# Performance work log

Measured on AMD Instinct MI355X. Metric: run time of the kernel, lower is better.

## Reference

```python
import jax, jax.numpy as jnp
import numpy as np
from jax import lax

NUM_CLASSES = 19
B, H, W = 4, 512, 512
IGNORE = 255
BLOCK = 16
MAX_N_RATIO = 0.01
LB_SMOOTH = 0.2
MAX_CLIP_DIST = 20.0
BORDER_FACTOR = 0.1
MAX_DIS = 1e5

# ---------- setup helpers (numpy, exact EDT matching scipy distance_transform_edt) ----------

def _edt(mask):
    """Exact Euclidean distance to nearest True pixel. mask: (H,W) bool."""
    Hm, Wm = mask.shape
    INF = 1e6
    g = np.where(mask, 0.0, INF).astype(np.float32)
    for j in range(1, Wm):
        g[:, j] = np.minimum(g[:, j], g[:, j - 1] + 1.0)
    for j in range(Wm - 2, -1, -1):
        g[:, j] = np.minimum(g[:, j], g[:, j + 1] + 1.0)
    gg = g * g  # (H,W) squared 1D row distances
    rows = np.arange(Hm, dtype=np.float32)
    out = np.empty((Hm, Wm), np.float32)
    CH = 64
    for s in range(0, Hm, CH):
        d2 = (rows[s:s + CH, None] - rows[None, :]) ** 2  # (CH,H)
        out[s:s + CH] = np.sqrt(np.min(d2[:, :, None] + gg[None, :, :], axis=1))
    return out


def _dist_maps(targets):
    """Replicates gtruth2boundary + dist_map_transform + relu(-dist): relu(EDT_to_boundary - 1)."""
    t = targets[:, 0]
    ud = np.zeros(t.shape, bool)
    lr = np.zeros(t.shape, bool)
    ud[:, :-1] = (t[:, 1:] - t[:, :-1]) != 0
    lr[:, :, :-1] = (t[:, :, 1:] - t[:, :, :-1]) != 0
    bnd = ud | lr | (t == IGNORE)
    out = np.zeros(t.shape, np.float32)
    for i in range(t.shape[0]):
        if bnd[i].any():
            out[i] = np.maximum(_edt(bnd[i]) - 1.0, 0.0)
    return out[:, None]  # (B,1,H,W)


def setup_inputs():
    key = jax.random.key(0)
    k1, k2 = jax.random.split(key)
    slices = jax.random.normal(k1, (B, NUM_CLASSES, H, W), jnp.float32)
    low = np.asarray(jax.random.randint(k2, (B, 1, H // BLOCK, W // BLOCK), 0, NUM_CLASSES))
    tgt = np.repeat(np.repeat(low, BLOCK, 2), BLOCK, 3).astype(np.int32)
    dist_maps = jnp.asarray(_dist_maps(tgt))
    return {"slices": slices, "dist_maps": dist_maps, "targets": jnp.asarray(tgt)}


# neighbor offset order from the torch code; index 8 is the center
_DX = [1, -1, 0, 0, -1, 1, -1, 1, 0]
_DY = [0, 0, -1, 1, 1, 1, -1, -1, 0]


def reference(slices, dist_maps, targets):
    Bc, C, Hc, Wc = slices.shape
    x = jnp.transpose(slices, (0, 2, 3, 1))               # (B,H,W,C)
    lsm = jax.nn.log_softmax(x, axis=-1)
    sm = jnp.exp(lsm)

    # ---- slices2boundary: per-pixel KL between adjacent pixels ----
    kl_ud = jnp.sum(sm[:, :-1] * (lsm[:, :-1] - lsm[:, 1:]), axis=-1)      # (B,H-1,W)
    kl_ud = jnp.pad(kl_ud, ((0, 0), (0, 1), (0, 0)))
    kl_lr = jnp.sum(sm[:, :, :-1] * (lsm[:, :, :-1] - lsm[:, :, 1:]), axis=-1)
    kl_lr = jnp.pad(kl_lr, ((0, 0), (0, 0), (0, 1)))
    klc = lax.stop_gradient(kl_ud + kl_lr)                # threshold is non-differentiable anyway

    max_N = Hc * Wc * MAX_N_RATIO
    eps = lax.while_loop(lambda e: jnp.sum(klc > e) > max_N,
                         lambda e: e * jnp.float32(1.2),
                         jnp.float32(1e-5))
    kb = (klc > eps).astype(jnp.float32)[:, None]          # (B,1,H,W)
    k3 = jnp.ones((1, 1, 3, 3), jnp.float32)
    dil = lax.conv_general_dilated(kb, k3, (1, 1), 'SAME',
                                   dimension_numbers=('NCHW', 'OIHW', 'NCHW'))
    pb = dil[:, 0] > 0                                     # pred boundary (B,H,W) bool

    # ---- get_orientation (dense masked version of the nonzero/gather code) ----
    pd = jnp.pad(dist_maps[:, 0], ((0, 0), (1, 1), (1, 1)), constant_values=MAX_DIS)
    lsm_p = lax.stop_gradient(jnp.pad(lsm, ((0, 0), (1, 1), (1, 1), (0, 0)), mode='edge'))
    sm_p = lax.stop_gradient(jnp.pad(sm, ((0, 0), (1, 1), (1, 1), (0, 0)), mode='edge'))

    dists, kls = [], []
    for dx, dy in zip(_DX, _DY):
        dists.append(pd[:, 1 + dx:1 + dx + Hc, 1 + dy:1 + dy + Wc])
        if dx != 0 or dy != 0:
            l_s = lsm_p[:, 1 + dx:1 + dx + Hc, 1 + dy:1 + dy + Wc]
            s_s = sm_p[:, 1 + dx:1 + dx + Hc, 1 + dy:1 + dy + Wc]
            # kl_div(center, neighbor) = softmax(nb) * (log_softmax(nb) - log_softmax(center))
            kls.append(jnp.sum(s_s * (l_s - lsm), axis=-1))
    dist9 = jnp.stack(dists, axis=-1)                      # (B,H,W,9)
    kl8 = jnp.stack(kls, axis=-1)                          # (B,H,W,8)

    dgt = jnp.argmin(dist9, axis=-1)                       # direction ground truth 0..8
    valid = pb & (dgt != 8)

    # label-smoothed softmax CE over the 8 directions (pytorch-loss LSSCE V1 semantics)
    lb_pos = 1.0 - LB_SMOOTH
    lb_neg = LB_SMOOTH / 8.0
    logq = jax.nn.log_softmax(kl8, axis=-1)
    onehot = jax.nn.one_hot(jnp.clip(dgt, 0, 7), 8, dtype=logq.dtype)
    smooth_lab = onehot * lb_pos + (1.0 - onehot) * lb_neg
    lsce = -jnp.sum(logq * smooth_lab, axis=-1)            # (B,H,W)

    w = jnp.minimum(dist_maps[:, 0], MAX_CLIP_DIST) / MAX_CLIP_DIST
    vm = valid.astype(jnp.float32)
    border_loss = jnp.sum(lsce * vm) * jnp.sum(w * vm)
    border_loss = jnp.where(jnp.sum(pb) > 1, border_loss, jnp.float32(0.0))

    # ---- target cross-entropy (reduction='none' then .sum()) ----
    tgt = targets[:, 0]
    ce = -jnp.take_along_axis(lsm, jnp.clip(tgt, 0, C - 1)[..., None], axis=-1)[..., 0]
    ce = jnp.where(tgt == IGNORE, 0.0, ce)
    target_loss = jnp.sum(ce)

    return BORDER_FACTOR * border_loss + target_loss
```

## Files before the change

### kernel.cpp

```cpp
#include <hip/hip_runtime.h>


#define NCLS 19
#define HH 512
#define WW 512
#define HWC (HH*WW)
#define CHW (NCLS*HWC)
#define NPIX (4*HWC)
#define NEPS 256
#define MAXDIS 100000.0f
#define LIST_CAP 32768
#define CNT_THRESH 2621u
#define SEG 4

#define O_LSE   0u
#define O_KLC   4194304u
#define O_TL    8388608u
#define O_CNT   8421376u
#define O_HIST  8425472u
#define O_LISTN 8426500u
#define O_SUMS  8426512u
#define O_EPS   8426528u
#define O_LIST  8426532u
#define MEMSET_OFF O_HIST
#define MEMSET_LEN 1056u

__global__ __launch_bounds__(256, 4) void kF_fused(
    const float* __restrict__ x, const int* __restrict__ tgt,
    float* __restrict__ lse_g, float* __restrict__ klc,
    unsigned int* __restrict__ hist, double* __restrict__ tl_part) {
  __shared__ float eps[NEPS];
  __shared__ unsigned int lh[NEPS + 1];
  __shared__ double sdce[256];
  int tid = threadIdx.x;
  for (int i = tid; i < NEPS + 1; i += 256) lh[i] = 0u;
  if (tid == 0) {
    float e = 1e-5f;
    for (int i = 0; i < NEPS; i++) { eps[i] = e; e *= 1.2f; }
  }
  __syncthreads();

  int bid = blockIdx.x;
  int b = bid >> 8;
  int r = bid & 255;
  int wh = r >> 7;
  int seg = r & 127;
  int h0 = seg * SEG;
  int w = (wh << 8) + tid;
  const float* xb = x + (size_t)b * CHW + w;
  int pbase = b * HWC + w;
  bool hasR = (w < WW - 1);
  int offR = hasR ? 1 : 0;

  float cur[NCLS];
  {
    const float* xr0 = xb + h0 * WW;
#pragma unroll
    for (int c = 0; c < NCLS; c++) cur[c] = xr0[(size_t)c * HWC];
  }
  float lse_cur;
  {
    float m = -1e30f;
#pragma unroll
    for (int c = 0; c < NCLS; c++) m = fmaxf(m, cur[c]);
    float s = 0.f;
#pragma unroll
    for (int c = 0; c < NCLS; c++) s += __expf(cur[c] - m);
    lse_cur = m + __logf(s);
  }
  double ce_acc = 0.0;

  for (int h = h0; h < h0 + SEG; ++h) {
    int p = pbase + h * WW;
    int row_n = (h < HH - 1) ? h + 1 : HH - 1;
    const float* xn = xb + row_n * WW;
    float nxt[NCLS];
#pragma unroll
    for (int c = 0; c < NCLS; c++) nxt[c] = xn[(size_t)c * HWC];
    const float* xc_ptr = xb + h * WW;
    float xr[NCLS];
#pragma unroll
    for (int c = 0; c < NCLS; c++) xr[c] = xc_ptr[(size_t)c * HWC + offR];

    int t = tgt[p];
    if (t != 255) {
      float xt = cur[0];
#pragma unroll
      for (int c = 1; c < NCLS; c++) xt = (t == c) ? cur[c] : xt;
      ce_acc += (double)(lse_cur - xt);
    }

    float lse_nxt;
    {
      float m = -1e30f;
#pragma unroll
      for (int c = 0; c < NCLS; c++) m = fmaxf(m, nxt[c]);
      float s = 0.f;
#pragma unroll
      for (int c = 0; c < NCLS; c++) s += __expf(nxt[c] - m);
      lse_nxt = m + __logf(s);
    }
    float lse_r;
    {
      float m = -1e30f;
#pragma unroll
      for (int c = 0; c < NCLS; c++) m = fmaxf(m, xr[c]);
      float s = 0.f;
#pragma unroll
      for (int c = 0; c < NCLS; c++) s += __expf(xr[c] - m);
      lse_r = m + __logf(s);
    }

    bool hasD = (h < HH - 1);
    float sD = 0.f, sR = 0.f;
#pragma unroll
    for (int c = 0; c < NCLS; c++) {
      float lmc = cur[c] - lse_cur;
      float pc = __expf(lmc);
      sD += pc * (lmc - (nxt[c] - lse_nxt));
      sR += pc * (lmc - (xr[c] - lse_r));
    }
    float kv = (hasD ? sD : 0.f) + (hasR ? sR : 0.f);
    klc[p] = kv;
    lse_g[p] = lse_cur;

    int lo = 0, hi = NEPS;
    while (lo < hi) {
      int mid = (lo + hi) >> 1;
      if (kv > eps[mid]) lo = mid + 1; else hi = mid;
    }
    atomicAdd(&lh[lo], 1u);

#pragma unroll
    for (int c = 0; c < NCLS; c++) cur[c] = nxt[c];
    lse_cur = lse_nxt;
  }

  sdce[tid] = ce_acc;
  __syncthreads();
  for (int o = 128; o > 0; o >>= 1) {
    if (tid < o) sdce[tid] += sdce[tid + o];
    __syncthreads();
  }
  if (tid == 0) tl_part[bid] = sdce[0];
  for (int i = tid; i < NEPS + 1; i += 256)
    if (lh[i]) atomicAdd(&hist[i], lh[i]);
}

__global__ void kC_eps(const unsigned int* __restrict__ hist, float* __restrict__ eps_final) {
  if (threadIdx.x == 0) {
    unsigned int cnt = 0;
    for (int i = 1; i <= NEPS; i++) cnt += hist[i];
    int K = 0;
    while (cnt > CNT_THRESH && K < NEPS - 1) {
      K++;
      cnt -= hist[K];
    }
    float e = 1e-5f;
    for (int i = 0; i < K; i++) e *= 1.2f;
    *eps_final = e;
  }
}

__global__ void kD1_compact(const float* __restrict__ klc, const float* __restrict__ epsp,
                            int* __restrict__ list, unsigned int* __restrict__ list_n,
                            unsigned int* __restrict__ cnt_part) {
  __shared__ unsigned int lcnt, lbase;
  __shared__ int lbuf[1024];
  int tid = threadIdx.x;
  if (tid == 0) lcnt = 0u;
  __syncthreads();
  float eps = *epsp;
  int base = blockIdx.x * 1024;
#pragma unroll
  for (int k = 0; k < 4; k++) {
    int p = base + k * 256 + tid;
    int b = p >> 18;
    int hw = p & (HWC - 1);
    int h = hw >> 9;
    int w = hw & 511;
    const float* kb = klc + b * HWC;
    bool pb = false;
#pragma unroll
    for (int dh = -1; dh <= 1; dh++)
#pragma unroll
      for (int dw = -1; dw <= 1; dw++) {
        int hh = h + dh, wn = w + dw;
        if (hh >= 0 && hh < HH && wn >= 0 && wn < WW)
          pb = pb || (kb[hh * WW + wn] > eps);
      }
    if (pb) {
      unsigned int idx = atomicAdd(&lcnt, 1u);
      lbuf[idx] = p;
    }
  }
  __syncthreads();
  if (tid == 0) {
    unsigned int c = lcnt;
    lbase = c ? atomicAdd(list_n, c) : 0u;
    cnt_part[blockIdx.x] = c;
  }
  __syncthreads();
  unsigned int c = lcnt, bo = lbase;
  for (unsigned int j = tid; j < c; j += 256) {
    unsigned int dst = bo + j;
    if (dst < LIST_CAP) list[dst] = lbuf[j];
  }
}

__global__ __launch_bounds__(256, 4) void kD2_border(
    const float* __restrict__ x, const float* __restrict__ lse,
    const float* __restrict__ dist, const int* __restrict__ list,
    const unsigned int* __restrict__ list_n,
    double* __restrict__ sums ) {
  const int DXc[9] = {1, -1, 0, 0, -1, 1, -1, 1, 0};
  const int DYc[9] = {0, 0, -1, 1, 1, 1, -1, -1, 0};
  __shared__ float skl[32][8];
  __shared__ float swl[4], sww[4];
  int tid = threadIdx.x;
  int gid = blockIdx.x * 256 + tid;
  int i = gid >> 3, k = gid & 7;
  unsigned int n = *list_n;
  if (n > LIST_CAP) n = LIST_CAP;
  float lsce = 0.f, wv = 0.f;
  bool act = (i < (int)n);
  int g = 8;
  float d8c = 0.f;
  int p = 0, b = 0, h = 0, w = 0, hw = 0;
  if (act) {
    p = list[i];
    b = p >> 18;
    hw = p & (HWC - 1);
    h = hw >> 9;
    w = hw & 511;
    const float* db = dist + b * HWC;
    float dv[9];
#pragma unroll
    for (int kk = 0; kk < 9; kk++) {
      int hh = h + DXc[kk], wn = w + DYc[kk];
      dv[kk] = (hh >= 0 && hh < HH && wn >= 0 && wn < WW) ? db[hh * WW + wn] : MAXDIS;
    }
    float dmin = dv[0];
    g = 0;
#pragma unroll
    for (int kk = 1; kk < 9; kk++)
      if (dv[kk] < dmin) { dmin = dv[kk]; g = kk; }
    d8c = dv[8];
    if (g != 8) {
      int dx = ((34898 >> (2 * k)) & 3) - 1;
      int dy = ((2693  >> (2 * k)) & 3) - 1;
      int hh = min(max(h + dx, 0), HH - 1);
      int wn = min(max(w + dy, 0), WW - 1);
      int hwn = hh * WW + wn;
      const float* xp = x + (size_t)b * CHW;
      float ln = lse[b * HWC + hwn];
      float lc = lse[p];
      float xnv[NCLS], xcv[NCLS];
#pragma unroll
      for (int c = 0; c < NCLS; c++) xnv[c] = xp[(size_t)c * HWC + hwn];
#pragma unroll
      for (int c = 0; c < NCLS; c++) xcv[c] = xp[(size_t)c * HWC + hw];
      float s = 0.f;
#pragma unroll
      for (int c = 0; c < NCLS; c++) {
        float lsn = xnv[c] - ln;
        s += __expf(lsn) * (lsn - (xcv[c] - lc));
      }
      skl[tid >> 3][k] = s;
    }
  }
  __syncthreads();
  if (act && g != 8 && k == 0) {
    float kl8[8];
#pragma unroll
    for (int kk = 0; kk < 8; kk++) kl8[kk] = skl[tid >> 3][kk];
    float m8 = kl8[0];
#pragma unroll
    for (int kk = 1; kk < 8; kk++) m8 = fmaxf(m8, kl8[kk]);
    float se = 0.f;
#pragma unroll
    for (int kk = 0; kk < 8; kk++) se += __expf(kl8[kk] - m8);
    float l8 = m8 + __logf(se);
    float sum_lq = 0.f, lq_g = 0.f;
#pragma unroll
    for (int kk = 0; kk < 8; kk++) {
      float lq = kl8[kk] - l8;
      sum_lq += lq;
      if (kk == g) lq_g = lq;
    }
    lsce = -(0.025f * sum_lq + 0.775f * lq_g);
    wv = fminf(d8c, 20.0f) * (1.0f / 20.0f);
  }
  float rl = lsce, rw = wv;
#pragma unroll
  for (int o = 32; o > 0; o >>= 1) {
    rl += __shfl_xor(rl, o);
    rw += __shfl_xor(rw, o);
  }
  if ((tid & 63) == 0) { swl[tid >> 6] = rl; sww[tid >> 6] = rw; }
  __syncthreads();
  if (tid == 0) {
    float tl = swl[0] + swl[1] + swl[2] + swl[3];
    float tw = sww[0] + sww[1] + sww[2] + sww[3];
    if (tl != 0.f || tw != 0.f) {
      atomicAdd(&sums[0], (double)tl);
      atomicAdd(&sums[1], (double)tw);
    }
  }
}

__global__ void kE_final(const double* __restrict__ tl_part, const unsigned int* __restrict__ cnt_part,
                         const double* __restrict__ sums, float* __restrict__ out) {
  __shared__ double sd[256];
  __shared__ unsigned int su[256];
  int t = threadIdx.x;
  double a = 0.0;
  for (int i = t; i < 1024; i += 256) a += tl_part[i];
  sd[t] = a;
  unsigned int c = 0;
  for (int i = t; i < 1024; i += 256) c += cnt_part[i];
  su[t] = c;
  __syncthreads();
  for (int o = 128; o > 0; o >>= 1) {
    if (t < o) { sd[t] += sd[t + o]; su[t] += su[t + o]; }
    __syncthreads();
  }
  if (t == 0) {
    double border = (su[0] > 1u) ? sums[0] * sums[1] : 0.0;
    out[0] = (float)(0.1 * border + sd[0]);
  }
}

extern "C" void kernel_launch(void* const* d_in, const int* in_sizes, int n_in,
                              void* d_out, int out_size, void* d_ws, size_t ws_size,
                              hipStream_t stream) {
  const float* x    = (const float*)d_in[0];
  const float* dist = (const float*)d_in[1];
  const int*   tgt  = (const int*)d_in[2];
  float* out = (float*)d_out;

  char* ws = (char*)d_ws;
  float*        lse      = (float*)(ws + O_LSE);
  float*        klc      = (float*)(ws + O_KLC);
  double*       tl_part  = (double*)(ws + O_TL);
  unsigned int* cnt_part = (unsigned int*)(ws + O_CNT);
  unsigned int* hist     = (unsigned int*)(ws + O_HIST);
  unsigned int* list_n   = (unsigned int*)(ws + O_LISTN);
  double*       sums     = (double*)(ws + O_SUMS);
  float*        eps_fin  = (float*)(ws + O_EPS);
  int*          list     = (int*)(ws + O_LIST);

  hipMemsetAsync(ws + MEMSET_OFF, 0, MEMSET_LEN, stream);

  kF_fused<<<1024, 256, 0, stream>>>(x, tgt, lse, klc, hist, tl_part);
  kC_eps<<<1, 64, 0, stream>>>(hist, eps_fin);
  kD1_compact<<<NPIX / 1024, 256, 0, stream>>>(klc, eps_fin, list, list_n, cnt_part);
  kD2_border<<<(LIST_CAP * 8) / 256, 256, 0, stream>>>(x, lse, dist, list, list_n, sums);
  kE_final<<<1, 256, 0, stream>>>(tl_part, cnt_part, sums, out);
}
```

Before: 190.3 us.

## Shuffle right-neighbor logits, fuse eps and final kernels into neighbors

In the main fused kernel, right-neighbor logits and their log-sum-exp now come from a wavefront shuffle of the current row instead of a second global load and a repeated reduction. Only the last lane of each wave still loads from memory. The eps-threshold kernel is folded into each compaction block, which redundantly scans a shared-memory copy of the histogram. The final reduction kernel is merged into the border kernel through a last-block atomic counter, which removes two launches. In the border kernel, the 9-way distance argmin is spread across 8 lanes with shuffles, and center-pixel logits are staged once in shared memory. The cost is redundant serial eps work in every compaction block and extra fences and atomics.

```diff
diff --git a/kernel.cpp b/kernel.cpp
--- a/kernel.cpp
+++ b/kernel.cpp
@@ -20,10 +20,10 @@
 #define O_HIST  8425472u
 #define O_LISTN 8426500u
 #define O_SUMS  8426512u
-#define O_EPS   8426528u
-#define O_LIST  8426532u
+#define O_CTR   8426528u
+#define O_LIST  8426536u
 #define MEMSET_OFF O_HIST
-#define MEMSET_LEN 1056u
+#define MEMSET_LEN 1060u
 
 __global__ __launch_bounds__(256, 4) void kF_fused(
     const float* __restrict__ x, const int* __restrict__ tgt,
@@ -51,12 +51,13 @@
   int pbase = b * HWC + w;
   bool hasR = (w < WW - 1);
   int offR = hasR ? 1 : 0;
+  bool edge = ((tid & 63) == 63);
 
   float cur[NCLS];
   {
-    const float* xr0 = xb + h0 * WW;
-#pragma unroll
-    for (int c = 0; c < NCLS; c++) cur[c] = xr0[(size_t)c * HWC];
+    const float* x0 = xb + h0 * WW;
+#pragma unroll
+    for (int c = 0; c < NCLS; c++) cur[c] = x0[(size_t)c * HWC];
   }
   float lse_cur;
   {
@@ -77,10 +78,23 @@
     float nxt[NCLS];
 #pragma unroll
     for (int c = 0; c < NCLS; c++) nxt[c] = xn[(size_t)c * HWC];
-    const float* xc_ptr = xb + h * WW;
+
     float xr[NCLS];
 #pragma unroll
-    for (int c = 0; c < NCLS; c++) xr[c] = xc_ptr[(size_t)c * HWC + offR];
+    for (int c = 0; c < NCLS; c++) xr[c] = __shfl_down(cur[c], 1);
+    float lse_r = __shfl_down(lse_cur, 1);
+    if (edge) {
+      const float* xc_ptr = xb + h * WW;
+#pragma unroll
+      for (int c = 0; c < NCLS; c++) xr[c] = xc_ptr[(size_t)c * HWC + offR];
+      float m = -1e30f;
+#pragma unroll
+      for (int c = 0; c < NCLS; c++) m = fmaxf(m, xr[c]);
+      float s = 0.f;
+#pragma unroll
+      for (int c = 0; c < NCLS; c++) s += __expf(xr[c] - m);
+      lse_r = m + __logf(s);
+    }
 
     int t = tgt[p];
     if (t != 255) {
@@ -99,16 +113,6 @@
 #pragma unroll
       for (int c = 0; c < NCLS; c++) s += __expf(nxt[c] - m);
       lse_nxt = m + __logf(s);
-    }
-    float lse_r;
-    {
-      float m = -1e30f;
-#pragma unroll
-      for (int c = 0; c < NCLS; c++) m = fmaxf(m, xr[c]);
-      float s = 0.f;
-#pragma unroll
-      for (int c = 0; c < NCLS; c++) s += __expf(xr[c] - m);
-      lse_r = m + __logf(s);
     }
 
     bool hasD = (h < HH - 1);
@@ -147,30 +151,31 @@
     if (lh[i]) atomicAdd(&hist[i], lh[i]);
 }
 
-__global__ void kC_eps(const unsigned int* __restrict__ hist, float* __restrict__ eps_final) {
-  if (threadIdx.x == 0) {
+__global__ void kD1_compact(const float* __restrict__ klc, const unsigned int* __restrict__ hist,
+                            int* __restrict__ list, unsigned int* __restrict__ list_n,
+                            unsigned int* __restrict__ cnt_part) {
+  __shared__ unsigned int shist[257];
+  __shared__ float seps;
+  __shared__ unsigned int lcnt, lbase;
+  __shared__ int lbuf[1024];
+  int tid = threadIdx.x;
+  for (int i = tid; i < 257; i += 256) shist[i] = hist[i];
+  if (tid == 0) lcnt = 0u;
+  __syncthreads();
+  if (tid == 0) {
     unsigned int cnt = 0;
-    for (int i = 1; i <= NEPS; i++) cnt += hist[i];
+    for (int i = 1; i <= NEPS; i++) cnt += shist[i];
     int K = 0;
     while (cnt > CNT_THRESH && K < NEPS - 1) {
       K++;
-      cnt -= hist[K];
+      cnt -= shist[K];
     }
     float e = 1e-5f;
     for (int i = 0; i < K; i++) e *= 1.2f;
-    *eps_final = e;
-  }
-}
-
-__global__ void kD1_compact(const float* __restrict__ klc, const float* __restrict__ epsp,
-                            int* __restrict__ list, unsigned int* __restrict__ list_n,
-                            unsigned int* __restrict__ cnt_part) {
-  __shared__ unsigned int lcnt, lbase;
-  __shared__ int lbuf[1024];
-  int tid = threadIdx.x;
-  if (tid == 0) lcnt = 0u;
-  __syncthreads();
-  float eps = *epsp;
+    seps = e;
+  }
+  __syncthreads();
+  float eps = seps;
   int base = blockIdx.x * 1024;
 #pragma unroll
   for (int k = 0; k < 4; k++) {
@@ -212,68 +217,78 @@
     const float* __restrict__ x, const float* __restrict__ lse,
     const float* __restrict__ dist, const int* __restrict__ list,
     const unsigned int* __restrict__ list_n,
-    double* __restrict__ sums ) {
-  const int DXc[9] = {1, -1, 0, 0, -1, 1, -1, 1, 0};
-  const int DYc[9] = {0, 0, -1, 1, 1, 1, -1, -1, 0};
+    double* __restrict__ sums ,
+    const double* __restrict__ tl_part, const unsigned int* __restrict__ cnt_part,
+    unsigned int* __restrict__ ctr, float* __restrict__ out) {
   __shared__ float skl[32][8];
+  __shared__ float sxc[32][20];
   __shared__ float swl[4], sww[4];
+  __shared__ int islast;
+  __shared__ double sd[256];
+  __shared__ unsigned int su[256];
   int tid = threadIdx.x;
   int gid = blockIdx.x * 256 + tid;
   int i = gid >> 3, k = gid & 7;
+  int px = tid >> 3;
   unsigned int n = *list_n;
   if (n > LIST_CAP) n = LIST_CAP;
+  bool act = (i < (int)n);
   float lsce = 0.f, wv = 0.f;
-  bool act = (i < (int)n);
-  int g = 8;
+  bool heavy = false;
+  int p = 0, b = 0, h = 0, w = 0, hw = 0, g = 8;
+  int dx = 0, dy = 0;
   float d8c = 0.f;
-  int p = 0, b = 0, h = 0, w = 0, hw = 0;
   if (act) {
     p = list[i];
     b = p >> 18;
     hw = p & (HWC - 1);
     h = hw >> 9;
     w = hw & 511;
+    dx = ((34898 >> (2 * k)) & 3) - 1;
+    dy = ((2693  >> (2 * k)) & 3) - 1;
     const float* db = dist + b * HWC;
-    float dv[9];
-#pragma unroll
-    for (int kk = 0; kk < 9; kk++) {
-      int hh = h + DXc[kk], wn = w + DYc[kk];
-      dv[kk] = (hh >= 0 && hh < HH && wn >= 0 && wn < WW) ? db[hh * WW + wn] : MAXDIS;
-    }
-    float dmin = dv[0];
-    g = 0;
-#pragma unroll
-    for (int kk = 1; kk < 9; kk++)
-      if (dv[kk] < dmin) { dmin = dv[kk]; g = kk; }
-    d8c = dv[8];
-    if (g != 8) {
-      int dx = ((34898 >> (2 * k)) & 3) - 1;
-      int dy = ((2693  >> (2 * k)) & 3) - 1;
-      int hh = min(max(h + dx, 0), HH - 1);
-      int wn = min(max(w + dy, 0), WW - 1);
-      int hwn = hh * WW + wn;
-      const float* xp = x + (size_t)b * CHW;
-      float ln = lse[b * HWC + hwn];
-      float lc = lse[p];
-      float xnv[NCLS], xcv[NCLS];
-#pragma unroll
-      for (int c = 0; c < NCLS; c++) xnv[c] = xp[(size_t)c * HWC + hwn];
-#pragma unroll
-      for (int c = 0; c < NCLS; c++) xcv[c] = xp[(size_t)c * HWC + hw];
-      float s = 0.f;
-#pragma unroll
-      for (int c = 0; c < NCLS; c++) {
-        float lsn = xnv[c] - ln;
-        s += __expf(lsn) * (lsn - (xcv[c] - lc));
-      }
-      skl[tid >> 3][k] = s;
-    }
-  }
-  __syncthreads();
-  if (act && g != 8 && k == 0) {
+    int hh = h + dx, wn = w + dy;
+    float dk = (hh >= 0 && hh < HH && wn >= 0 && wn < WW) ? db[hh * WW + wn] : MAXDIS;
+    d8c = db[hw];
+    float v = dk;
+    int idx = k;
+#pragma unroll
+    for (int off = 1; off < 8; off <<= 1) {
+      float vo = __shfl_xor(v, off);
+      int io = __shfl_xor(idx, off);
+      if (vo < v || (vo == v && io < idx)) { v = vo; idx = io; }
+    }
+    g = (d8c < v) ? 8 : idx;
+    heavy = (g != 8);
+  }
+  if (heavy) {
+    const float* xp = x + (size_t)b * CHW;
+    for (int c = k; c < NCLS; c += 8) sxc[px][c] = xp[(size_t)c * HWC + hw];
+  }
+  __syncthreads();
+  if (heavy) {
+    int hh = min(max(h + dx, 0), HH - 1);
+    int wn = min(max(w + dy, 0), WW - 1);
+    int hwn = hh * WW + wn;
+    const float* xp = x + (size_t)b * CHW;
+    float ln = lse[b * HWC + hwn];
+    float lc = lse[p];
+    float xnv[NCLS];
+#pragma unroll
+    for (int c = 0; c < NCLS; c++) xnv[c] = xp[(size_t)c * HWC + hwn];
+    float s = 0.f;
+#pragma unroll
+    for (int c = 0; c < NCLS; c++) {
+      float lsn = xnv[c] - ln;
+      s += __expf(lsn) * (lsn - (sxc[px][c] - lc));
+    }
+    skl[px][k] = s;
+  }
+  __syncthreads();
+  if (heavy && k == 0) {
     float kl8[8];
 #pragma unroll
-    for (int kk = 0; kk < 8; kk++) kl8[kk] = skl[tid >> 3][kk];
+    for (int kk = 0; kk < 8; kk++) kl8[kk] = skl[px][kk];
     float m8 = kl8[0];
 #pragma unroll
     for (int kk = 1; kk < 8; kk++) m8 = fmaxf(m8, kl8[kk]);
@@ -306,28 +321,30 @@
       atomicAdd(&sums[0], (double)tl);
       atomicAdd(&sums[1], (double)tw);
     }
-  }
-}
-
-__global__ void kE_final(const double* __restrict__ tl_part, const unsigned int* __restrict__ cnt_part,
-                         const double* __restrict__ sums, float* __restrict__ out) {
-  __shared__ double sd[256];
-  __shared__ unsigned int su[256];
-  int t = threadIdx.x;
-  double a = 0.0;
-  for (int i = t; i < 1024; i += 256) a += tl_part[i];
-  sd[t] = a;
-  unsigned int c = 0;
-  for (int i = t; i < 1024; i += 256) c += cnt_part[i];
-  su[t] = c;
-  __syncthreads();
-  for (int o = 128; o > 0; o >>= 1) {
-    if (t < o) { sd[t] += sd[t + o]; su[t] += su[t + o]; }
+    __threadfence();
+    unsigned int old = atomicAdd(ctr, 1u);
+    islast = (old == gridDim.x - 1) ? 1 : 0;
+  }
+  __syncthreads();
+  if (islast) {
+    __threadfence();
+    double a = 0.0;
+    for (int j = tid; j < 1024; j += 256) a += tl_part[j];
+    sd[tid] = a;
+    unsigned int c = 0;
+    for (int j = tid; j < 1024; j += 256) c += cnt_part[j];
+    su[tid] = c;
     __syncthreads();
-  }
-  if (t == 0) {
-    double border = (su[0] > 1u) ? sums[0] * sums[1] : 0.0;
-    out[0] = (float)(0.1 * border + sd[0]);
+    for (int o = 128; o > 0; o >>= 1) {
+      if (tid < o) { sd[tid] += sd[tid + o]; su[tid] += su[tid + o]; }
+      __syncthreads();
+    }
+    if (tid == 0) {
+      double s0 = atomicAdd(&sums[0], 0.0);
+      double s1 = atomicAdd(&sums[1], 0.0);
+      double border = (su[0] > 1u) ? s0 * s1 : 0.0;
+      out[0] = (float)(0.1 * border + sd[0]);
+    }
   }
 }
 
@@ -347,14 +364,13 @@
   unsigned int* hist     = (unsigned int*)(ws + O_HIST);
   unsigned int* list_n   = (unsigned int*)(ws + O_LISTN);
   double*       sums     = (double*)(ws + O_SUMS);
-  float*        eps_fin  = (float*)(ws + O_EPS);
+  unsigned int* ctr      = (unsigned int*)(ws + O_CTR);
   int*          list     = (int*)(ws + O_LIST);
 
   hipMemsetAsync(ws + MEMSET_OFF, 0, MEMSET_LEN, stream);
 
   kF_fused<<<1024, 256, 0, stream>>>(x, tgt, lse, klc, hist, tl_part);
-  kC_eps<<<1, 64, 0, stream>>>(hist, eps_fin);
-  kD1_compact<<<NPIX / 1024, 256, 0, stream>>>(klc, eps_fin, list, list_n, cnt_part);
-  kD2_border<<<(LIST_CAP * 8) / 256, 256, 0, stream>>>(x, lse, dist, list, list_n, sums);
-  kE_final<<<1, 256, 0, stream>>>(tl_part, cnt_part, sums, out);
+  kD1_compact<<<NPIX / 1024, 256, 0, stream>>>(klc, hist, list, list_n, cnt_part);
+  kD2_border<<<(LIST_CAP * 8) / 256, 256, 0, stream>>>(x, lse, dist, list, list_n, sums,
+                                                       tl_part, cnt_part, ctr, out);
 }
```

Measured after the change: 209.5 us. 10.1% more time.

## Share right-neighbor logits via warp shuffle and fold eps selection into compaction

Applied to the files above, without the earlier changes.

The fused kernel now gets the right neighbor's logits and log-sum-exp from the adjacent lane with __shfl_down. Only lanes at wavefront edges reload from global memory and recompute the LSE, which removes a redundant 19-channel load and exp pass per pixel. The single-thread eps-selection kernel is dropped, and every compaction block rebuilds eps from the histogram in shared memory, saving one launch at the cost of a serial scan repeated in each block. The edge test assumes 64-wide wavefronts.

```diff
diff --git a/kernel.cpp b/kernel.cpp
--- a/kernel.cpp
+++ b/kernel.cpp
@@ -20,7 +20,6 @@
 #define O_HIST  8425472u
 #define O_LISTN 8426500u
 #define O_SUMS  8426512u
-#define O_EPS   8426528u
 #define O_LIST  8426532u
 #define MEMSET_OFF O_HIST
 #define MEMSET_LEN 1056u
@@ -51,12 +50,13 @@
   int pbase = b * HWC + w;
   bool hasR = (w < WW - 1);
   int offR = hasR ? 1 : 0;
+  bool edge = ((tid & 63) == 63);
 
   float cur[NCLS];
   {
-    const float* xr0 = xb + h0 * WW;
-#pragma unroll
-    for (int c = 0; c < NCLS; c++) cur[c] = xr0[(size_t)c * HWC];
+    const float* x0 = xb + h0 * WW;
+#pragma unroll
+    for (int c = 0; c < NCLS; c++) cur[c] = x0[(size_t)c * HWC];
   }
   float lse_cur;
   {
@@ -77,10 +77,23 @@
     float nxt[NCLS];
 #pragma unroll
     for (int c = 0; c < NCLS; c++) nxt[c] = xn[(size_t)c * HWC];
-    const float* xc_ptr = xb + h * WW;
+
     float xr[NCLS];
 #pragma unroll
-    for (int c = 0; c < NCLS; c++) xr[c] = xc_ptr[(size_t)c * HWC + offR];
+    for (int c = 0; c < NCLS; c++) xr[c] = __shfl_down(cur[c], 1);
+    float lse_r = __shfl_down(lse_cur, 1);
+    if (edge) {
+      const float* xc_ptr = xb + h * WW;
+#pragma unroll
+      for (int c = 0; c < NCLS; c++) xr[c] = xc_ptr[(size_t)c * HWC + offR];
+      float m = -1e30f;
+#pragma unroll
+      for (int c = 0; c < NCLS; c++) m = fmaxf(m, xr[c]);
+      float s = 0.f;
+#pragma unroll
+      for (int c = 0; c < NCLS; c++) s += __expf(xr[c] - m);
+      lse_r = m + __logf(s);
+    }
 
     int t = tgt[p];
     if (t != 255) {
@@ -99,16 +112,6 @@
 #pragma unroll
       for (int c = 0; c < NCLS; c++) s += __expf(nxt[c] - m);
       lse_nxt = m + __logf(s);
-    }
-    float lse_r;
-    {
-      float m = -1e30f;
-#pragma unroll
-      for (int c = 0; c < NCLS; c++) m = fmaxf(m, xr[c]);
-      float s = 0.f;
-#pragma unroll
-      for (int c = 0; c < NCLS; c++) s += __expf(xr[c] - m);
-      lse_r = m + __logf(s);
     }
 
     bool hasD = (h < HH - 1);
@@ -147,30 +150,31 @@
     if (lh[i]) atomicAdd(&hist[i], lh[i]);
 }
 
-__global__ void kC_eps(const unsigned int* __restrict__ hist, float* __restrict__ eps_final) {
-  if (threadIdx.x == 0) {
+__global__ void kD1_compact(const float* __restrict__ klc, const unsigned int* __restrict__ hist,
+                            int* __restrict__ list, unsigned int* __restrict__ list_n,
+                            unsigned int* __restrict__ cnt_part) {
+  __shared__ unsigned int shist[257];
+  __shared__ float seps;
+  __shared__ unsigned int lcnt, lbase;
+  __shared__ int lbuf[1024];
+  int tid = threadIdx.x;
+  for (int i = tid; i < 257; i += 256) shist[i] = hist[i];
+  if (tid == 0) lcnt = 0u;
+  __syncthreads();
+  if (tid == 0) {
     unsigned int cnt = 0;
-    for (int i = 1; i <= NEPS; i++) cnt += hist[i];
+    for (int i = 1; i <= NEPS; i++) cnt += shist[i];
     int K = 0;
     while (cnt > CNT_THRESH && K < NEPS - 1) {
       K++;
-      cnt -= hist[K];
+      cnt -= shist[K];
     }
     float e = 1e-5f;
     for (int i = 0; i < K; i++) e *= 1.2f;
-    *eps_final = e;
-  }
-}
-
-__global__ void kD1_compact(const float* __restrict__ klc, const float* __restrict__ epsp,
-                            int* __restrict__ list, unsigned int* __restrict__ list_n,
-                            unsigned int* __restrict__ cnt_part) {
-  __shared__ unsigned int lcnt, lbase;
-  __shared__ int lbuf[1024];
-  int tid = threadIdx.x;
-  if (tid == 0) lcnt = 0u;
-  __syncthreads();
-  float eps = *epsp;
+    seps = e;
+  }
+  __syncthreads();
+  float eps = seps;
   int base = blockIdx.x * 1024;
 #pragma unroll
   for (int k = 0; k < 4; k++) {
@@ -347,14 +351,12 @@
   unsigned int* hist     = (unsigned int*)(ws + O_HIST);
   unsigned int* list_n   = (unsigned int*)(ws + O_LISTN);
   double*       sums     = (double*)(ws + O_SUMS);
-  float*        eps_fin  = (float*)(ws + O_EPS);
   int*          list     = (int*)(ws + O_LIST);
 
   hipMemsetAsync(ws + MEMSET_OFF, 0, MEMSET_LEN, stream);
 
   kF_fused<<<1024, 256, 0, stream>>>(x, tgt, lse, klc, hist, tl_part);
-  kC_eps<<<1, 64, 0, stream>>>(hist, eps_fin);
-  kD1_compact<<<NPIX / 1024, 256, 0, stream>>>(klc, eps_fin, list, list_n, cnt_part);
+  kD1_compact<<<NPIX / 1024, 256, 0, stream>>>(klc, hist, list, list_n, cnt_part);
   kD2_border<<<(LIST_CAP * 8) / 256, 256, 0, stream>>>(x, lse, dist, list, list_n, sums);
   kE_final<<<1, 256, 0, stream>>>(tl_part, cnt_part, sums, out);
 }
```

Result: no change. 192.7 us (+1.3%).
